# Kernel tuning notes

Measured on AMD Instinct MI355X. Metric: run time of the kernel, lower is better.

## Reference

```python
import jax, jax.numpy as jnp
from jax import lax
import numpy as np

IN, COV, H1, H2, OUT_LEN = 64, 256, 512, 512, 90
B, T = 128, 365

def setup_inputs() -> dict:
    key = jax.random.key(0)
    ks = jax.random.split(key, 12)
    s = 0.05
    return {
        "input": jax.random.normal(ks[0], (B, T, IN), jnp.float32),
        "covar": jax.random.normal(ks[1], (B, COV), jnp.float32),
        "W_ih1": jax.random.normal(ks[2], (4 * H1, IN + COV), jnp.float32) * s,
        "W_hh1": jax.random.normal(ks[3], (4 * H1, H1), jnp.float32) * s,
        "b1":    jax.random.normal(ks[4], (4 * H1,), jnp.float32) * s,
        "W_ih2": jax.random.normal(ks[5], (4 * H2, H1 + COV), jnp.float32) * s,
        "W_hh2": jax.random.normal(ks[6], (4 * H2, H2), jnp.float32) * s,
        "b2":    jax.random.normal(ks[7], (4 * H2,), jnp.float32) * s,
        "W_fc":  jax.random.normal(ks[8], (1, H2), jnp.float32) * s,
        "b_fc":  jax.random.normal(ks[9], (1,), jnp.float32) * s,
    }

def _lstm_cell(h, c, gates, W_hh):
    # gates: precomputed input projection + bias, shape [B, 4H]
    g = gates + h @ W_hh.T
    i, f, gg, o = jnp.split(g, 4, axis=-1)  # torch gate order i,f,g,o
    c = jax.nn.sigmoid(f) * c + jax.nn.sigmoid(i) * jnp.tanh(gg)
    h = jax.nn.sigmoid(o) * jnpy_tanh(c) if False else jax.nn.sigmoid(o) * jnp.tanh(c)
    return h, c

def reference(input, covar, W_ih1, W_hh1, b1, W_ih2, W_hh2, b2, W_fc, b_fc):
    Bb, Tt, _ = input.shape
    dtype = input.dtype
    # ---- encoder LSTM over concatenated [input, covar] ----
    x1 = jnp.concatenate([input, jnp.broadcast_to(covar[:, None, :], (Bb, Tt, covar.shape[1]))], axis=2)
    proj1 = jnp.einsum('bti,gi->tbg', x1, W_ih1) + b1  # [T, B, 4H1]
    h0 = jnp.zeros((Bb, W_hh1.shape[1]), dtype)
    def step1(carry, pt):
        h, c = carry
        h, c = _lstm_cell(h, c, pt, W_hh1)
        return (h, c), None
    (h_enc, _), _ = lax.scan(step1, (h0, h0), proj1)
    h_enc = jax.nn.relu(h_enc)  # [B, H1]
    # ---- decoder LSTM: constant input [relu(h_enc), covar] repeated OUT_LEN steps ----
    dec_in = jnp.concatenate([h_enc, covar], axis=1)
    proj2 = dec_in @ W_ih2.T + b2  # [B, 4H2], same every step
    h0d = jnp.zeros((Bb, W_hh2.shape[1]), dtype)
    def step2(carry, _):
        h, c = carry
        h, c = _lstm_cell(h, c, proj2, W_hh2)
        return (h, c), h
    _, hs = lax.scan(step2, (h0d, h0d), None, length=OUT_LEN)  # [OUT_LEN, B, H2]
    out2 = jax.nn.relu(hs.transpose(1, 0, 2))  # [B, OUT_LEN, H2]
    out = out2 @ W_fc.T + b_fc  # [B, OUT_LEN, 1]
    return jnp.squeeze(out, axis=-1)  # [B, OUT_LEN]
```

## Files before the change

### kernel.cpp

```cpp
#include <hip/hip_runtime.h>


namespace {
constexpr int B = 128, T = 365, IN = 64, COV = 256, H = 512, OUTL = 90;
constexpr int GB = 8;
constexpr int GJ = 32;
constexpr int NWG = GB * GJ;
constexpr int NT = 256;
constexpr int BS = B / GB;
constexpr int HU = H / GJ;
constexpr int NR = 4 * HU;
constexpr int NSLOT_H = 64;
constexpr int NSLOT = 72;
}

using ull = unsigned long long;
typedef __attribute__((ext_vector_type(8))) short short8;
typedef __attribute__((ext_vector_type(4))) short short4v;
typedef __attribute__((ext_vector_type(8))) _Float16 half8;
typedef __attribute__((ext_vector_type(4))) float f32x4;

__device__ unsigned int g_h[2][B][H];
__device__ float g_part[OUTL][GJ][B];
__device__ __align__(256) int g_flag[GB][32];

__device__ __forceinline__ float sigfast(float x) {
  return __builtin_amdgcn_rcpf(1.0f + __expf(-x));
}
__device__ __forceinline__ float tanhfast(float x) {
  return 1.0f - 2.0f * __builtin_amdgcn_rcpf(__expf(2.0f * x) + 1.0f);
}

__device__ __forceinline__ float4 fma4(float4 a, float4 b, float4 c) {
  c.x = fmaf(a.x, b.x, c.x); c.y = fmaf(a.y, b.y, c.y);
  c.z = fmaf(a.z, b.z, c.z); c.w = fmaf(a.w, b.w, c.w);
  return c;
}
__device__ __forceinline__ float hsum4(float4 a) { return (a.x + a.y) + (a.z + a.w); }

__device__ __forceinline__ unsigned int pack_split(float v) {
  _Float16 hi = (_Float16)v;
  _Float16 lo = (_Float16)(v - (float)hi);
  return ((unsigned int)__builtin_bit_cast(unsigned short, hi) << 16) |
         (unsigned int)__builtin_bit_cast(unsigned short, lo);
}
__device__ __forceinline__ float unpack_split(unsigned int u) {
  _Float16 hi = __builtin_bit_cast(_Float16, (unsigned short)(u >> 16));
  _Float16 lo = __builtin_bit_cast(_Float16, (unsigned short)(u & 0xFFFFu));
  return (float)hi + (float)lo;
}

__device__ __forceinline__ void cvt8(const float* src, half8& hi, half8& lo) {
  float4 p0 = ((const float4*)src)[0], p1 = ((const float4*)src)[1];
  float f[8] = {p0.x, p0.y, p0.z, p0.w, p1.x, p1.y, p1.z, p1.w};
#pragma unroll
  for (int j = 0; j < 8; ++j) {
    _Float16 h_ = (_Float16)f[j];
    hi[j] = h_;
    lo[j] = (_Float16)(f[j] - (float)h_);
  }
}

__global__ void __launch_bounds__(256) k_init() {
  int t = threadIdx.x;
  if (t < GB * 32) g_flag[t >> 5][t & 31] = 0;
}

__global__ void __launch_bounds__(NT, 1) k_lstm(
    const float* __restrict__ input, const float* __restrict__ covar,
    const float* __restrict__ W_ih1, const float* __restrict__ W_hh1,
    const float* __restrict__ b1,    const float* __restrict__ W_ih2,
    const float* __restrict__ W_hh2, const float* __restrict__ b2,
    const float* __restrict__ W_fc) {
  __shared__ __align__(16) short bH[BS][NSLOT * 8];
  __shared__ __align__(16) short bL[BS][NSLOT * 8];
  __shared__ float pb_lds[NR][17];
  __shared__ float aux[4][16];

  const int tid = threadIdx.x;
  const int gb  = blockIdx.x & (GB - 1);
  const int gj  = blockIdx.x >> 3;
  const int bg0 = gb * BS;
  const int j0  = gj * HU;

  const int lane  = tid & 63;
  const int wv    = tid >> 6;
  const int rows0 = wv * 16;
  const int ra    = rows0 + (lane & 15);
  const int b_l   = lane & 15;
  const int cc    = lane >> 4;
  const int x7    = lane & 7;
  const int u_l   = wv * 4 + cc;

  const int bl  = tid >> 4;
  const int sg  = tid & 15;
  const int bt  = tid & 15;
  const int rt  = tid >> 4;

  const int growA = (ra & 3) * H + j0 + (ra >> 2);

  half8 wA[16], wLo[16];
  half8 xA[2],  xLo[2];

  auto stage_whh_regs = [&](const float* Whh) {
    const float* base = Whh + (size_t)growA * H + cc * 8;
#pragma unroll
    for (int kb = 0; kb < 16; ++kb) cvt8(base + kb * 32, wA[kb], wLo[kb]);
  };

  auto load_x_regs = [&](int tn, float4& p) {
    p = *(const float4*)(input + ((size_t)(bg0 + bl) * T + tn) * IN + sg * 4);
  };
  auto stage_x_regs = [&](float4 p) {
    float f[4] = {p.x, p.y, p.z, p.w};
    short4v hi, lo;
#pragma unroll
    for (int j = 0; j < 4; ++j) {
      _Float16 h_ = (_Float16)f[j];
      hi[j] = __builtin_bit_cast(short, h_);
      lo[j] = __builtin_bit_cast(short, (_Float16)(f[j] - (float)h_));
    }
    const int s2 = (NSLOT_H + (sg >> 1)) ^ (bl & 7);
    *(short4v*)&bH[bl][s2 * 8 + (sg & 1) * 4] = hi;
    *(short4v*)&bL[bl][s2 * 8 + (sg & 1) * 4] = lo;
  };

  auto gbar = [&](int nb, bool with_x, float4 xp, int gp_ot) {
    __syncthreads();
    if (tid == 0)
      __hip_atomic_store(&g_flag[gb][gj], nb, __ATOMIC_RELAXED,
                         __HIP_MEMORY_SCOPE_AGENT);
    if (with_x) stage_x_regs(xp);
    if (gp_ot >= 0 && tid < 16)
      g_part[gp_ot][gj][bg0 + tid] =
          aux[0][tid] + aux[1][tid] + aux[2][tid] + aux[3][tid];
    if (tid < 32) {
      while (__hip_atomic_load(&g_flag[gb][tid], __ATOMIC_RELAXED,
                               __HIP_MEMORY_SCOPE_AGENT) < nb)
        __builtin_amdgcn_s_sleep(1);
    }
    __syncthreads();
  };

  auto load_h = [&](int par, ull (&tmp)[16]) {
    const ull* hr = (const ull*)&g_h[par][bg0 + bl][0];
#pragma unroll
    for (int i = 0; i < 16; ++i)
      tmp[i] = __hip_atomic_load(hr + sg + 16 * i, __ATOMIC_RELAXED,
                                 __HIP_MEMORY_SCOPE_AGENT);
  };
  auto commit_h = [&](ull (&tmp)[16]) {
#pragma unroll
    for (int i = 0; i < 16; ++i) {
      const int m = sg + 16 * i;
      const int s2 = (m >> 2) ^ (bl & 7);
      const int p = m & 3;
      const unsigned u0 = (unsigned)tmp[i], u1 = (unsigned)(tmp[i] >> 32);
      ((unsigned*)&bH[bl][s2 * 8])[p] = (u0 >> 16) | (u1 & 0xFFFF0000u);
      ((unsigned*)&bL[bl][s2 * 8])[p] = (u0 & 0xFFFFu) | (u1 << 16);
    }
  };

  auto mfma_kb = [&](int kb, half8 ah, half8 al,
                     f32x4& aA, f32x4& aB, f32x4& aC) {
    const int s2 = (kb * 4 + cc) ^ x7;
    const half8 bh = __builtin_bit_cast(half8, *(const short8*)&bH[b_l][s2 * 8]);
    const half8 bo = __builtin_bit_cast(half8, *(const short8*)&bL[b_l][s2 * 8]);
    aA = __builtin_amdgcn_mfma_f32_16x16x32_f16(ah, bh, aA, 0, 0, 0);
    aB = __builtin_amdgcn_mfma_f32_16x16x32_f16(ah, bo, aB, 0, 0, 0);
    aC = __builtin_amdgcn_mfma_f32_16x16x32_f16(al, bh, aC, 0, 0, 0);
  };

  auto wrow = [&](int r) { return (r & 3) * H + j0 + (r >> 2); };

  stage_whh_regs(W_hh1);
  {
    const float* base = W_ih1 + (size_t)growA * (IN + COV) + cc * 8;
#pragma unroll
    for (int xk = 0; xk < 2; ++xk) cvt8(base + xk * 32, xA[xk], xLo[xk]);
  }
  {
    const float4* cv = (const float4*)(covar + (size_t)(bg0 + bt) * COV);
    float accr[4] = {0.f, 0.f, 0.f, 0.f};
    const float4* wp[4];
#pragma unroll
    for (int rr = 0; rr < 4; ++rr)
      wp[rr] = (const float4*)(W_ih1 + (size_t)wrow(rt + rr * 16) * (IN + COV) + IN);
    for (int k = 0; k < COV / 4; ++k) {
      const float4 cvk = cv[k];
#pragma unroll
      for (int rr = 0; rr < 4; ++rr) {
        const float4 w = wp[rr][k];
        accr[rr] += cvk.x * w.x + cvk.y * w.y + cvk.z * w.z + cvk.w * w.w;
      }
    }
#pragma unroll
    for (int rr = 0; rr < 4; ++rr)
      pb_lds[rt + rr * 16][bt] = accr[rr] + b1[wrow(rt + rr * 16)];
  }
  {
    float4 p;
    load_x_regs(0, p);
    stage_x_regs(p);
  }
  __syncthreads();

  float pb4[4];
#pragma unroll
  for (int q = 0; q < 4; ++q) pb4[q] = pb_lds[rows0 + cc * 4 + q][b_l];

  float c_state = 0.0f;

  auto cellp = [&](const f32x4& acc) -> float {
    const float gi = acc[0] + pb4[0];
    const float gf = acc[1] + pb4[1];
    const float gg = acc[2] + pb4[2];
    const float go = acc[3] + pb4[3];
    c_state = sigfast(gf) * c_state + sigfast(gi) * tanhfast(gg);
    return sigfast(go) * tanhfast(c_state);
  };

  for (int t = 0; t < T; ++t) {
    ull tmp[16];
    if (t > 0) load_h(t & 1, tmp);
    f32x4 aA = {0.f, 0.f, 0.f, 0.f}, aB = aA, aC = aA;
#pragma unroll
    for (int xk = 0; xk < 2; ++xk)
      mfma_kb(16 + xk, xA[xk], xLo[xk], aA, aB, aC);
    if (t > 0) commit_h(tmp);
    __syncthreads();
    if (t > 0) {
#pragma unroll
      for (int kb = 0; kb < 16; ++kb)
        mfma_kb(kb, wA[kb], wLo[kb], aA, aB, aC);
    }
    f32x4 acc;
#pragma unroll
    for (int q = 0; q < 4; ++q) acc[q] = aA[q] + aB[q] + aC[q];
    float hv = cellp(acc);
    if (t == T - 1) hv = fmaxf(hv, 0.0f);
    __hip_atomic_store(&g_h[(t + 1) & 1][bg0 + b_l][j0 + u_l], pack_split(hv),
                       __ATOMIC_RELAXED, __HIP_MEMORY_SCOPE_AGENT);
    float4 xp = {0.f, 0.f, 0.f, 0.f};
    const bool havex = (t + 1 < T);
    if (havex) load_x_regs(t + 1, xp);
    gbar(t + 1, havex, xp, -1);
  }

  {
    const ull* hb = (const ull*)&g_h[1][bg0 + bt][0];
    const float* wr[4];
    float accr[4] = {0.f, 0.f, 0.f, 0.f};
#pragma unroll
    for (int rr = 0; rr < 4; ++rr)
      wr[rr] = W_ih2 + (size_t)wrow(rt + rr * 16) * (H + COV);
    for (int m = 0; m < H / 2; ++m) {
      const ull v = __hip_atomic_load(hb + m, __ATOMIC_RELAXED,
                                      __HIP_MEMORY_SCOPE_AGENT);
      const float h0 = unpack_split((unsigned)v);
      const float h1 = unpack_split((unsigned)(v >> 32));
#pragma unroll
      for (int rr = 0; rr < 4; ++rr)
        accr[rr] += h0 * wr[rr][2 * m] + h1 * wr[rr][2 * m + 1];
    }
    {
      const float4* cv = (const float4*)(covar + (size_t)(bg0 + bt) * COV);
      for (int k = 0; k < COV / 4; ++k) {
        const float4 cvk = cv[k];
#pragma unroll
        for (int rr = 0; rr < 4; ++rr) {
          const float4 w = ((const float4*)wr[rr])[H / 4 + k];
          accr[rr] += cvk.x * w.x + cvk.y * w.y + cvk.z * w.z + cvk.w * w.w;
        }
      }
    }
#pragma unroll
    for (int rr = 0; rr < 4; ++rr)
      pb_lds[rt + rr * 16][bt] = accr[rr] + b2[wrow(rt + rr * 16)];
  }
  stage_whh_regs(W_hh2);
  c_state = 0.0f;
  {
    float4 dummy = {0.f, 0.f, 0.f, 0.f};
    gbar(T + 1, false, dummy, -1);
  }

#pragma unroll
  for (int q = 0; q < 4; ++q) pb4[q] = pb_lds[rows0 + cc * 4 + q][b_l];
  const float wfc = W_fc[j0 + u_l];

  for (int ot = 0; ot < OUTL; ++ot) {
    if (ot > 0) {
      ull tmp[16];
      load_h(ot & 1, tmp);
      commit_h(tmp);
    }
    __syncthreads();
    f32x4 aA = {0.f, 0.f, 0.f, 0.f}, aB = aA, aC = aA;
    if (ot > 0) {
#pragma unroll
      for (int kb = 0; kb < 16; ++kb)
        mfma_kb(kb, wA[kb], wLo[kb], aA, aB, aC);
    }
    f32x4 acc;
#pragma unroll
    for (int q = 0; q < 4; ++q) acc[q] = aA[q] + aB[q] + aC[q];
    const float hv = cellp(acc);
    __hip_atomic_store(&g_h[(ot + 1) & 1][bg0 + b_l][j0 + u_l], pack_split(hv),
                       __ATOMIC_RELAXED, __HIP_MEMORY_SCOPE_AGENT);
    float fcv = fmaxf(hv, 0.0f) * wfc;
    fcv += __shfl_xor(fcv, 16);
    fcv += __shfl_xor(fcv, 32);
    if (lane < 16) aux[wv][lane] = fcv;
    float4 dummy = {0.f, 0.f, 0.f, 0.f};
    gbar(T + 2 + ot, false, dummy, ot);
  }
}

__global__ void __launch_bounds__(256) k_reduce(const float* __restrict__ b_fc,
                                                float* __restrict__ out) {
  int id = blockIdx.x * 256 + threadIdx.x;
  if (id >= B * OUTL) return;
  int b = id / OUTL, ot = id - b * OUTL;
  float s = b_fc[0];
#pragma unroll 8
  for (int g = 0; g < GJ; ++g) s += g_part[ot][g][b];
  out[id] = s;
}

extern "C" void kernel_launch(void* const* d_in, const int* in_sizes, int n_in,
                              void* d_out, int out_size, void* d_ws, size_t ws_size,
                              hipStream_t stream) {
  (void)in_sizes; (void)n_in; (void)d_ws; (void)ws_size; (void)out_size;
  const float* input = (const float*)d_in[0];
  const float* covar = (const float*)d_in[1];
  const float* W_ih1 = (const float*)d_in[2];
  const float* W_hh1 = (const float*)d_in[3];
  const float* b1    = (const float*)d_in[4];
  const float* W_ih2 = (const float*)d_in[5];
  const float* W_hh2 = (const float*)d_in[6];
  const float* b2    = (const float*)d_in[7];
  const float* W_fc  = (const float*)d_in[8];
  const float* b_fc  = (const float*)d_in[9];

  k_init<<<dim3(1), dim3(256), 0, stream>>>();
  k_lstm<<<dim3(NWG), dim3(NT), 0, stream>>>(input, covar, W_ih1, W_hh1, b1,
                                             W_ih2, W_hh2, b2, W_fc);
  k_reduce<<<dim3((B * OUTL + 255) / 256), dim3(256), 0, stream>>>(
      b_fc, (float*)d_out);
}
```

Baseline: 1.395 ms.

## Speculatively prefetch hidden state during grid barrier with epoch-tagged validation

Each hidden-state word now carries an epoch bit in its least significant bit. Workgroups issue the global load of the next step's h while spinning in the grid barrier, then validate the epoch bits after the barrier and reload only if stale. This hides global load latency behind barrier waiting. The cost is one bit of low-half precision, a larger init kernel, and a possible extra reload.

```diff
diff --git a/kernel.cpp b/kernel.cpp
--- a/kernel.cpp
+++ b/kernel.cpp
@@ -36,7 +36,6 @@
   c.z = fmaf(a.z, b.z, c.z); c.w = fmaf(a.w, b.w, c.w);
   return c;
 }
-__device__ __forceinline__ float hsum4(float4 a) { return (a.x + a.y) + (a.z + a.w); }
 
 __device__ __forceinline__ unsigned int pack_split(float v) {
   _Float16 hi = (_Float16)v;
@@ -62,8 +61,14 @@
 }
 
 __global__ void __launch_bounds__(256) k_init() {
-  int t = threadIdx.x;
-  if (t < GB * 32) g_flag[t >> 5][t & 31] = 0;
+  const int id = blockIdx.x * 256 + threadIdx.x;
+  unsigned* h0 = &g_h[0][0][0];
+  if (id < B * H) {
+    h0[id] = 0u;
+    h0[B * H + id] = 1u;
+  }
+  if (blockIdx.x == 0 && threadIdx.x < GB * 32)
+    g_flag[threadIdx.x >> 5][threadIdx.x & 31] = 0;
 }
 
 __global__ void __launch_bounds__(NT, 1) k_lstm(
@@ -125,11 +130,32 @@
     *(short4v*)&bL[bl][s2 * 8 + (sg & 1) * 4] = lo;
   };
 
-  auto gbar = [&](int nb, bool with_x, float4 xp, int gp_ot) {
+  ull spec[16];
+  auto load_h = [&](int par, ull (&tmp)[16]) {
+    const ull* hr = (const ull*)&g_h[par][bg0 + bl][0];
+#pragma unroll
+    for (int i = 0; i < 16; ++i)
+      tmp[i] = __hip_atomic_load(hr + sg + 16 * i, __ATOMIC_RELAXED,
+                                 __HIP_MEMORY_SCOPE_AGENT);
+  };
+  auto commit_h = [&](ull (&tmp)[16]) {
+#pragma unroll
+    for (int i = 0; i < 16; ++i) {
+      const int m = sg + 16 * i;
+      const int s2 = (m >> 2) ^ (bl & 7);
+      const int p = m & 3;
+      const unsigned u0 = (unsigned)tmp[i], u1 = (unsigned)(tmp[i] >> 32);
+      ((unsigned*)&bH[bl][s2 * 8])[p] = (u0 >> 16) | (u1 & 0xFFFF0000u);
+      ((unsigned*)&bL[bl][s2 * 8])[p] = (u0 & 0xFFFFu) | (u1 << 16);
+    }
+  };
+
+  auto gbar = [&](int nb, bool with_x, float4 xp, int gp_ot, int spec_par) {
     __syncthreads();
     if (tid == 0)
       __hip_atomic_store(&g_flag[gb][gj], nb, __ATOMIC_RELAXED,
                          __HIP_MEMORY_SCOPE_AGENT);
+    if (spec_par >= 0) load_h(spec_par, spec);
     if (with_x) stage_x_regs(xp);
     if (gp_ot >= 0 && tid < 16)
       g_part[gp_ot][gj][bg0 + tid] =
@@ -142,23 +168,18 @@
     __syncthreads();
   };
 
-  auto load_h = [&](int par, ull (&tmp)[16]) {
-    const ull* hr = (const ull*)&g_h[par][bg0 + bl][0];
+  auto validate_h = [&](int par, unsigned e) {
+    unsigned bad = 0;
 #pragma unroll
     for (int i = 0; i < 16; ++i)
-      tmp[i] = __hip_atomic_load(hr + sg + 16 * i, __ATOMIC_RELAXED,
-                                 __HIP_MEMORY_SCOPE_AGENT);
-  };
-  auto commit_h = [&](ull (&tmp)[16]) {
-#pragma unroll
-    for (int i = 0; i < 16; ++i) {
-      const int m = sg + 16 * i;
-      const int s2 = (m >> 2) ^ (bl & 7);
-      const int p = m & 3;
-      const unsigned u0 = (unsigned)tmp[i], u1 = (unsigned)(tmp[i] >> 32);
-      ((unsigned*)&bH[bl][s2 * 8])[p] = (u0 >> 16) | (u1 & 0xFFFF0000u);
-      ((unsigned*)&bL[bl][s2 * 8])[p] = (u0 & 0xFFFFu) | (u1 << 16);
-    }
+      bad |= ((unsigned)spec[i] ^ e) | ((unsigned)(spec[i] >> 32) ^ e);
+    if (bad & 1u) load_h(par, spec);
+  };
+
+  auto store_h = [&](int wb, unsigned we, float hv) {
+    const unsigned u = (pack_split(hv) & ~1u) | we;
+    __hip_atomic_store(&g_h[wb][bg0 + b_l][j0 + u_l], u,
+                       __ATOMIC_RELAXED, __HIP_MEMORY_SCOPE_AGENT);
   };
 
   auto mfma_kb = [&](int kb, half8 ah, half8 al,
@@ -221,13 +242,12 @@
   };
 
   for (int t = 0; t < T; ++t) {
-    ull tmp[16];
-    if (t > 0) load_h(t & 1, tmp);
+    if (t > 0) validate_h(t & 1, (unsigned)((t >> 1) & 1));
     f32x4 aA = {0.f, 0.f, 0.f, 0.f}, aB = aA, aC = aA;
 #pragma unroll
     for (int xk = 0; xk < 2; ++xk)
       mfma_kb(16 + xk, xA[xk], xLo[xk], aA, aB, aC);
-    if (t > 0) commit_h(tmp);
+    if (t > 0) commit_h(spec);
     __syncthreads();
     if (t > 0) {
 #pragma unroll
@@ -239,12 +259,12 @@
     for (int q = 0; q < 4; ++q) acc[q] = aA[q] + aB[q] + aC[q];
     float hv = cellp(acc);
     if (t == T - 1) hv = fmaxf(hv, 0.0f);
-    __hip_atomic_store(&g_h[(t + 1) & 1][bg0 + b_l][j0 + u_l], pack_split(hv),
-                       __ATOMIC_RELAXED, __HIP_MEMORY_SCOPE_AGENT);
+    store_h((t + 1) & 1, (unsigned)(((t + 1) >> 1) & 1), hv);
     float4 xp = {0.f, 0.f, 0.f, 0.f};
     const bool havex = (t + 1 < T);
     if (havex) load_x_regs(t + 1, xp);
-    gbar(t + 1, havex, xp, -1);
+    gbar(t + 1, havex, xp, -1,
+         (t + 1 < T) ? ((t + 1) & 1) : -1);
   }
 
   {
@@ -282,7 +302,7 @@
   c_state = 0.0f;
   {
     float4 dummy = {0.f, 0.f, 0.f, 0.f};
-    gbar(T + 1, false, dummy, -1);
+    gbar(T + 1, false, dummy, -1, -1);
   }
 
 #pragma unroll
@@ -290,11 +310,9 @@
   const float wfc = W_fc[j0 + u_l];
 
   for (int ot = 0; ot < OUTL; ++ot) {
-    if (ot > 0) {
-      ull tmp[16];
-      load_h(ot & 1, tmp);
-      commit_h(tmp);
-    }
+    const int sc = T + ot;
+    if (ot > 0) validate_h(sc & 1, (unsigned)((sc >> 1) & 1));
+    if (ot > 0) commit_h(spec);
     __syncthreads();
     f32x4 aA = {0.f, 0.f, 0.f, 0.f}, aB = aA, aC = aA;
     if (ot > 0) {
@@ -306,14 +324,14 @@
 #pragma unroll
     for (int q = 0; q < 4; ++q) acc[q] = aA[q] + aB[q] + aC[q];
     const float hv = cellp(acc);
-    __hip_atomic_store(&g_h[(ot + 1) & 1][bg0 + b_l][j0 + u_l], pack_split(hv),
-                       __ATOMIC_RELAXED, __HIP_MEMORY_SCOPE_AGENT);
+    store_h((sc + 1) & 1, (unsigned)(((sc + 1) >> 1) & 1), hv);
     float fcv = fmaxf(hv, 0.0f) * wfc;
     fcv += __shfl_xor(fcv, 16);
     fcv += __shfl_xor(fcv, 32);
     if (lane < 16) aux[wv][lane] = fcv;
     float4 dummy = {0.f, 0.f, 0.f, 0.f};
-    gbar(T + 2 + ot, false, dummy, ot);
+    gbar(T + 2 + ot, false, dummy, ot,
+         (ot + 1 < OUTL) ? ((sc + 1) & 1) : -1);
   }
 }
 
@@ -343,7 +361,7 @@
   const float* W_fc  = (const float*)d_in[8];
   const float* b_fc  = (const float*)d_in[9];
 
-  k_init<<<dim3(1), dim3(256), 0, stream>>>();
+  k_init<<<dim3((B * H + 255) / 256), dim3(256), 0, stream>>>();
   k_lstm<<<dim3(NWG), dim3(NT), 0, stream>>>(input, covar, W_ih1, W_hh1, b1,
                                              W_ih2, W_hh2, b2, W_fc);
   k_reduce<<<dim3((B * OUTL + 255) / 256), dim3(256), 0, stream>>>(
```

New measurement: 1.819 ms. 30.4% more time.
